# Optimization experiments

Hardware: AMD Instinct MI355X
Metric: run time of the kernel (lower is better)

The kernel has to match this reference:

```python
import jax, jax.numpy as jnp
import numpy as np

B, S, E = 2, 2048, 2048
H, KV, HD = 16, 4, 128  # num_heads, num_kv_heads, head_dim
G = H // KV             # query heads per kv head
ROPE_BASE = 10000.0


def rope_tables(dim, maxlen):
    freqs = 1.0 / ROPE_BASE ** (jnp.arange(0, dim, 2, dtype=jnp.float32) / dim)
    t = jnp.arange(maxlen, dtype=jnp.float32)
    f = jnp.outer(t, freqs)  # (maxlen, dim//2)
    return jnp.cos(f), jnp.sin(f)


def apply_rope(x, cos, sin):
    # x: (..., seq, heads, head_dim); interleaved-pair rotation
    s_len = x.shape[-3]
    c = cos[:s_len][:, None, :]
    s = sin[:s_len][:, None, :]
    x1 = x[..., ::2]
    x2 = x[..., 1::2]
    return jnp.stack([x1 * c - x2 * s, x1 * s + x2 * c], axis=-1).reshape(x.shape)


def setup_inputs() -> dict:
    key = jax.random.key(0)
    kx, kq, kk, kv, ko = jax.random.split(key, 5)
    x = jax.random.normal(kx, (B, S, E), dtype=jnp.float32)
    Wq = jax.random.normal(kq, (E, H * HD), dtype=jnp.float32) * 0.02
    Wk = jax.random.normal(kk, (E, KV * HD), dtype=jnp.float32) * 0.02
    Wv = jax.random.normal(kv, (E, KV * HD), dtype=jnp.float32) * 0.02
    Wo = jax.random.normal(ko, (H * HD, E), dtype=jnp.float32) * 0.02
    mask = jnp.tril(jnp.ones((S, S), dtype=bool))[None, None]  # causal (1,1,S,S)
    return {"x": x, "Wq": Wq, "Wk": Wk, "Wv": Wv, "Wo": Wo, "mask": mask}


def reference(x, Wq, Wk, Wv, Wo, mask):
    b, s, _ = x.shape
    cos, sin = rope_tables(HD, s)
    q = (x @ Wq).reshape(b, s, H, HD)
    k = (x @ Wk).reshape(b, s, KV, HD)
    v = (x @ Wv).reshape(b, s, KV, HD)
    q = apply_rope(q, cos, sin)
    k = apply_rope(k, cos, sin)
    if G > 1:
        k = jnp.repeat(k, G, axis=2)  # (b, s, H, HD)
        v = jnp.repeat(v, G, axis=2)
    q = jnp.transpose(q, (0, 2, 1, 3))  # (b, H, s, HD)
    k = jnp.transpose(k, (0, 2, 1, 3))
    v = jnp.transpose(v, (0, 2, 1, 3))
    scale = jnp.sqrt(jnp.float32(HD)).astype(q.dtype)
    scores = jnp.einsum("bhqd,bhkd->bhqk", q, k) / scale
    scores = jnp.where(mask, scores, jnp.finfo(scores.dtype).min)
    attn = jax.nn.softmax(scores, axis=-1)
    out = jnp.einsum("bhqk,bhkd->bhqd", attn, v)
    out = jnp.transpose(out, (0, 2, 1, 3)).reshape(b, s, H * HD)
    return out @ Wo
```

## Files before the change

### kernel.cpp

```cpp
#include <hip/hip_runtime.h>
#include <hip/hip_bf16.h>
#include <cstdint>

#define B_ 2
#define S_ 2048
#define E_ 2048
#define H_ 16
#define KV_ 4
#define HD_ 128
#define BS_ (B_*S_)
#define QKV_LD 3072
#define SM_SCALE 0.08838834764831845f
#define SC_LOG2E 0.1275424488538497f

typedef __attribute__((ext_vector_type(8))) __bf16 bf16x8;
typedef __attribute__((ext_vector_type(4))) float  floatx4;

__device__ __forceinline__ unsigned short f2bf(float f) {
  union { float f; unsigned u; } v; v.f = f;
  unsigned r = v.u + 0x7fffu + ((v.u >> 16) & 1u);
  return (unsigned short)(r >> 16);
}
__device__ __forceinline__ float bf2f(unsigned short u) {
  union { unsigned u; float f; } v; v.u = ((unsigned)u) << 16; return v.f;
}
__device__ __forceinline__ unsigned pack_bf16x2(float a, float b) {
  union { __hip_bfloat162 h; unsigned u; } v;
  v.h = __float22bfloat162_rn(make_float2(a, b));
  return v.u;
}

__device__ __forceinline__ void async_cp16(const void* g, void* l) {
  __builtin_amdgcn_global_load_lds(
      (const __attribute__((address_space(1))) void*)g,
      (__attribute__((address_space(3))) void*)l, 16, 0, 0);
}

__global__ __launch_bounds__(256)
void cvt_bf16(const float* __restrict__ src, unsigned short* __restrict__ dst,
              int n4) {
  int idx = blockIdx.x * 256 + threadIdx.x;
  if (idx >= n4) return;
  float4 v = *(const float4*)(src + (size_t)idx * 4);
  ushort4 o;
  o.x = f2bf(v.x); o.y = f2bf(v.y); o.z = f2bf(v.z); o.w = f2bf(v.w);
  *(ushort4*)(dst + (size_t)idx * 4) = o;
}

__global__ __launch_bounds__(256)
void cvt_bf16_t(const float* __restrict__ src, unsigned short* __restrict__ dst,
                int N, int dld, int noff) {
  __shared__ float tile[64 * 65];
  const int t = threadIdx.x;
  const int bk = blockIdx.y * 64, bn = blockIdx.x * 64;
  const int r = t >> 2, cg = t & 3;
#pragma unroll
  for (int i = 0; i < 4; ++i) {
    int c = cg * 16 + i * 4;
    float4 v = *(const float4*)(src + (size_t)(bk + r) * N + bn + c);
    tile[r * 65 + c] = v.x; tile[r * 65 + c + 1] = v.y;
    tile[r * 65 + c + 2] = v.z; tile[r * 65 + c + 3] = v.w;
  }
  __syncthreads();
  const int nl = t >> 2, kg = t & 3;
  union { unsigned short u[16]; uint4 q[2]; } o;
#pragma unroll
  for (int j = 0; j < 16; ++j)
    o.u[j] = f2bf(tile[(kg * 16 + j) * 65 + nl]);
  unsigned short* dp = dst + (size_t)(noff + bn + nl) * dld + bk + kg * 16;
  *(uint4*)(dp) = o.q[0];
  *(uint4*)(dp + 8) = o.q[1];
}

__global__ __launch_bounds__(256)
void rope_kernel(unsigned short* __restrict__ qkv) {
  const int PPR = 1280;
  int idx = blockIdx.x * 256 + threadIdx.x;
  if (idx >= BS_ * PPR) return;
  int row = idx / PPR, p = idx - row * PPR;
  int col = (p < 1024) ? (2 * p) : (2048 + 2 * (p - 1024));
  int d = p & 63;
  int s = row & (S_ - 1);
  float freq = expf(-(float)d * 0.14391156831212787f);
  float ang = (float)s * freq;
  float c = cosf(ang), sn = sinf(ang);
  unsigned short* ptr = qkv + (size_t)row * QKV_LD + col;
  float x1 = bf2f(ptr[0]), x2 = bf2f(ptr[1]);
  ptr[0] = f2bf(x1 * c - x2 * sn);
  ptr[1] = f2bf(x1 * sn + x2 * c);
}

__global__ __launch_bounds__(256)
void vtrans_kernel(const unsigned short* __restrict__ qkv,
                   unsigned short* __restrict__ vt) {
  __shared__ unsigned short tile[64 * 72];
  const int tid = threadIdx.x;
  const int s0 = blockIdx.x * 64;
  const int g = blockIdx.y >> 1;
  const int hh = (blockIdx.y & 1) * 64;
  const int b = g >> 2, kvh = g & 3;
#pragma unroll
  for (int i = 0; i < 2; ++i) {
    int chunk = tid + i * 256;
    int r = chunk >> 3, c = (chunk & 7) * 8;
    uint4 v = *(const uint4*)(qkv + (size_t)(b * S_ + s0 + r) * QKV_LD + 2560 + kvh * HD_ + hh + c);
    *(uint4*)(tile + r * 72 + c) = v;
  }
  __syncthreads();
#pragma unroll
  for (int i = 0; i < 2; ++i) {
    int chunk = tid + i * 256;
    int hdr = chunk >> 3, sc = (chunk & 7) * 8;
    union { unsigned short u[8]; uint4 v; } t;
#pragma unroll
    for (int j = 0; j < 8; ++j) t.u[j] = tile[(sc + j) * 72 + hdr];
    *(uint4*)(vt + (size_t)(g * HD_ + hh + hdr) * S_ + s0 + sc) = t.v;
  }
}

template<bool OUT_BF16>
__global__ __launch_bounds__(256, 2)
void gemm_tn(const unsigned short* __restrict__ A,
             const unsigned short* __restrict__ BT,
             void* __restrict__ C, int M, int N, int K) {
  __shared__ unsigned short Ash[128 * 32];
  __shared__ unsigned short Bsh[128 * 32];
  const int tid = threadIdx.x;
  const int l = tid & 63;
  const int l16 = l & 15, l4 = l >> 4;
  const int wave = tid >> 6;
  const int wm = (wave >> 1) * 64, wn = (wave & 1) * 64;
  const int bm = blockIdx.y * 128, bn = blockIdx.x * 128;

  const int srow = l >> 2;
  const int sg = (((l & 3) - (l >> 4)) & 3) * 8;

  floatx4 acc[4][4] = {};

  for (int kb = 0; kb < K; kb += 32) {
    __syncthreads();
#pragma unroll
    for (int i = 0; i < 2; ++i) {
      int cc = wave + i * 4;
      async_cp16(A + (size_t)(bm + 16 * cc + srow) * K + kb + sg, &Ash[cc * 512]);
      async_cp16(BT + (size_t)(bn + 16 * cc + srow) * K + kb + sg, &Bsh[cc * 512]);
    }
    __syncthreads();
    bf16x8 af[4], bf[4];
#pragma unroll
    for (int t = 0; t < 4; ++t) {
      int row = wm + t * 16 + l16;
      int s = (l4 + (l16 >> 2)) & 3;
      af[t] = *(const bf16x8*)(Ash + row * 32 + s * 8);
    }
#pragma unroll
    for (int t = 0; t < 4; ++t) {
      int row = wn + t * 16 + l16;
      int s = (l4 + (l16 >> 2)) & 3;
      bf[t] = *(const bf16x8*)(Bsh + row * 32 + s * 8);
    }
#pragma unroll
    for (int tm = 0; tm < 4; ++tm)
#pragma unroll
      for (int tn = 0; tn < 4; ++tn)
        acc[tm][tn] = __builtin_amdgcn_mfma_f32_16x16x32_bf16(af[tm], bf[tn], acc[tm][tn], 0, 0, 0);
  }
#pragma unroll
  for (int tm = 0; tm < 4; ++tm)
#pragma unroll
    for (int tn = 0; tn < 4; ++tn)
#pragma unroll
      for (int r = 0; r < 4; ++r) {
        int row = bm + wm + tm * 16 + l4 * 4 + r;
        int col = bn + wn + tn * 16 + l16;
        float v = acc[tm][tn][r];
        if (OUT_BF16) ((unsigned short*)C)[(size_t)row * N + col] = f2bf(v);
        else          ((float*)C)[(size_t)row * N + col] = v;
      }
}

__global__ __launch_bounds__(256, 2)
void gqa_attention(const unsigned short* __restrict__ qkv,
                   const unsigned short* __restrict__ vt,
                   unsigned short* __restrict__ out) {
  __shared__ unsigned short Ksh[2][32 * 128];
  __shared__ unsigned short Vsh[2][128 * 32];

  const int tid = threadIdx.x, l = tid & 63, wave = tid >> 6;
  const int l16 = l & 15, l4 = l >> 4;
  const int g = blockIdx.x, b = g >> 2, kvh = g & 3;
  const int h = kvh * 4 + wave;

  const int k_subrow = l >> 4;
  const int v_subrow = l >> 2;
  const int gv = (((l & 3) - (l >> 4)) & 3) * 8;

  const int t = 63 - (int)blockIdx.y;
  const int qt = t * 32;
  const int nch = t + 1;

  bf16x8 qfA[4], qfB[4];
  {
    const unsigned short* qpA = qkv + (size_t)(b * S_ + qt + l16) * QKV_LD + h * HD_;
    const unsigned short* qpB = qpA + (size_t)16 * QKV_LD;
#pragma unroll
    for (int c = 0; c < 4; ++c) {
      qfA[c] = *(const bf16x8*)(qpA + c * 32 + l4 * 8);
      qfB[c] = *(const bf16x8*)(qpB + c * 32 + l4 * 8);
    }
  }
  asm volatile("s_waitcnt vmcnt(0)" ::: "memory");

  const unsigned short* kp[2];
  const unsigned short* vp[2];
#pragma unroll
  for (int i = 0; i < 2; ++i) {
    int cc = wave + i * 4;
    int krow = 4 * cc + k_subrow;
    int gk = (((l & 15) - krow) & 15) * 8;
    kp[i] = qkv + (size_t)(b * S_ + krow) * QKV_LD + 2048 + kvh * HD_ + gk;
    vp[i] = vt + (size_t)(g * HD_ + 16 * cc + v_subrow) * S_ + gv;
  }

#pragma unroll
  for (int i = 0; i < 2; ++i) {
    int cc = wave + i * 4;
    async_cp16(kp[i], &Ksh[0][cc * 512]);
    async_cp16(vp[i], &Vsh[0][cc * 512]);
  }

  float lsumA = 0.f, lsumB = 0.f;
  floatx4 accA[8] = {}, accB[8] = {};

  for (int it = 0; it < nch; ++it) {
    const int cur = it & 1;
    asm volatile("s_barrier" ::: "memory");
    {
      const int kb2 = (it + 1 < nch) ? (it + 1) * 32 : 0;
      const int ko = kb2 * QKV_LD;
#pragma unroll
      for (int i = 0; i < 2; ++i) {
        int cc = wave + i * 4;
        async_cp16(kp[i] + ko, &Ksh[cur ^ 1][cc * 512]);
        async_cp16(vp[i] + kb2, &Vsh[cur ^ 1][cc * 512]);
      }
    }
    asm volatile("s_waitcnt vmcnt(4)\n\ts_barrier" ::: "memory");

    floatx4 saccA[2] = {}, saccB[2] = {};
    __builtin_amdgcn_s_setprio(1);
#pragma unroll
    for (int half = 0; half < 2; ++half) {
      int krow = half * 16 + l16;
#pragma unroll
      for (int c = 0; c < 4; ++c) {
        int s = (c * 4 + l4 + l16) & 15;
        bf16x8 kf = *(const bf16x8*)(&Ksh[cur][krow * 128 + s * 8]);
        saccA[half] = __builtin_amdgcn_mfma_f32_16x16x32_bf16(kf, qfA[c], saccA[half], 0, 0, 0);
        saccB[half] = __builtin_amdgcn_mfma_f32_16x16x32_bf16(kf, qfB[c], saccB[half], 0, 0, 0);
      }
    }
    __builtin_amdgcn_s_setprio(0);

    float pA[8], pB[8];
    if (it == nch - 1) {
#pragma unroll
      for (int half = 0; half < 2; ++half)
#pragma unroll
        for (int r = 0; r < 4; ++r) {
          int kk = half * 16 + l4 * 4 + r;
          float vA = fminf(saccA[half][r] * SC_LOG2E, 80.f);
          if (kk > l16) vA = -3e38f;
          float eA = exp2f(vA);
          pA[half * 4 + r] = eA; lsumA += eA;
          float vB = fminf(saccB[half][r] * SC_LOG2E, 80.f);
          if (half == 1 && (l4 * 4 + r) > l16) vB = -3e38f;
          float eB = exp2f(vB);
          pB[half * 4 + r] = eB; lsumB += eB;
        }
    } else {
#pragma unroll
      for (int half = 0; half < 2; ++half)
#pragma unroll
        for (int r = 0; r < 4; ++r) {
          float eA = exp2f(fminf(saccA[half][r] * SC_LOG2E, 80.f));
          pA[half * 4 + r] = eA; lsumA += eA;
          float eB = exp2f(fminf(saccB[half][r] * SC_LOG2E, 80.f));
          pB[half * 4 + r] = eB; lsumB += eB;
        }
    }

    unsigned a0 = pack_bf16x2(pA[0], pA[1]);
    unsigned a1 = pack_bf16x2(pA[2], pA[3]);
    unsigned a2 = pack_bf16x2(pA[4], pA[5]);
    unsigned a3 = pack_bf16x2(pA[6], pA[7]);
    asm("v_permlane32_swap_b32 %0, %1" : "+v"(a0), "+v"(a2));
    asm("v_permlane16_swap_b32 %0, %1" : "+v"(a0), "+v"(a2));
    asm("v_permlane32_swap_b32 %0, %1" : "+v"(a1), "+v"(a3));
    asm("v_permlane16_swap_b32 %0, %1" : "+v"(a1), "+v"(a3));
    unsigned b0 = pack_bf16x2(pB[0], pB[1]);
    unsigned b1 = pack_bf16x2(pB[2], pB[3]);
    unsigned b2 = pack_bf16x2(pB[4], pB[5]);
    unsigned b3 = pack_bf16x2(pB[6], pB[7]);
    asm("v_permlane32_swap_b32 %0, %1" : "+v"(b0), "+v"(b2));
    asm("v_permlane16_swap_b32 %0, %1" : "+v"(b0), "+v"(b2));
    asm("v_permlane32_swap_b32 %0, %1" : "+v"(b1), "+v"(b3));
    asm("v_permlane16_swap_b32 %0, %1" : "+v"(b1), "+v"(b3));
    union { unsigned w[4]; bf16x8 v8; } punA, punB;
    punA.w[0] = a0; punA.w[1] = a1; punA.w[2] = a2; punA.w[3] = a3;
    punB.w[0] = b0; punB.w[1] = b1; punB.w[2] = b2; punB.w[3] = b3;
    const bf16x8 pfA = punA.v8;
    const bf16x8 pfB = punB.v8;

    __builtin_amdgcn_s_setprio(1);
#pragma unroll
    for (int u = 0; u < 8; ++u) {
      int row = u * 16 + l16;
      int s = (l4 + (l16 >> 2)) & 3;
      bf16x8 vf = *(const bf16x8*)(&Vsh[cur][row * 32 + s * 8]);
      accA[u] = __builtin_amdgcn_mfma_f32_16x16x32_bf16(vf, pfA, accA[u], 0, 0, 0);
      accB[u] = __builtin_amdgcn_mfma_f32_16x16x32_bf16(vf, pfB, accB[u], 0, 0, 0);
    }
    __builtin_amdgcn_s_setprio(0);
  }

  lsumA += __shfl_xor(lsumA, 16, 64);
  lsumA += __shfl_xor(lsumA, 32, 64);
  lsumB += __shfl_xor(lsumB, 16, 64);
  lsumB += __shfl_xor(lsumB, 32, 64);
  float invA = 1.0f / lsumA;
  float invB = 1.0f / lsumB;
  unsigned short* opA = out + (size_t)(b * S_ + qt + l16) * 2048 + h * HD_;
  unsigned short* opB = opA + (size_t)16 * 2048;
#pragma unroll
  for (int u = 0; u < 8; ++u) {
    uint2 oA, oB;
    oA.x = pack_bf16x2(accA[u][0] * invA, accA[u][1] * invA);
    oA.y = pack_bf16x2(accA[u][2] * invA, accA[u][3] * invA);
    *(uint2*)(opA + u * 16 + l4 * 4) = oA;
    oB.x = pack_bf16x2(accB[u][0] * invB, accB[u][1] * invB);
    oB.y = pack_bf16x2(accB[u][2] * invB, accB[u][3] * invB);
    *(uint2*)(opB + u * 16 + l4 * 4) = oB;
  }
}

extern "C" void kernel_launch(void* const* d_in, const int* in_sizes, int n_in,
                              void* d_out, int out_size, void* d_ws, size_t ws_size,
                              hipStream_t stream) {
  const float* x  = (const float*)d_in[0];
  const float* Wq = (const float*)d_in[1];
  const float* Wk = (const float*)d_in[2];
  const float* Wv = (const float*)d_in[3];
  const float* Wo = (const float*)d_in[4];
  float* out = (float*)d_out;

  char* ws = (char*)d_ws;
  unsigned short* xb    = (unsigned short*)(ws);
  unsigned short* wqkvT = (unsigned short*)(ws + 16777216);
  unsigned short* woT   = (unsigned short*)(ws + 29360128);
  unsigned short* qkv   = (unsigned short*)(ws + 37748736);
  unsigned short* attn  = (unsigned short*)(ws + 62914560);
  unsigned short* vt    = (unsigned short*)(ws);

  cvt_bf16<<<(4096 * 2048 / 4 + 255) / 256, 256, 0, stream>>>(x, xb, 4096 * 2048 / 4);
  cvt_bf16_t<<<dim3(32, 32), 256, 0, stream>>>(Wq, wqkvT, 2048, 2048, 0);
  cvt_bf16_t<<<dim3(8, 32),  256, 0, stream>>>(Wk, wqkvT, 512,  2048, 2048);
  cvt_bf16_t<<<dim3(8, 32),  256, 0, stream>>>(Wv, wqkvT, 512,  2048, 2560);
  cvt_bf16_t<<<dim3(32, 32), 256, 0, stream>>>(Wo, woT,  2048, 2048, 0);

  gemm_tn<true><<<dim3(24, 32), 256, 0, stream>>>(xb, wqkvT, qkv, 4096, 3072, 2048);
  rope_kernel<<<(4096 * 1280 + 255) / 256, 256, 0, stream>>>(qkv);
  vtrans_kernel<<<dim3(32, 16), 256, 0, stream>>>(qkv, vt);
  gqa_attention<<<dim3(8, 64), 256, 0, stream>>>(qkv, vt, attn);
  gemm_tn<false><<<dim3(16, 32), 256, 0, stream>>>(attn, woT, out, 4096, 2048, 2048);
}
```

Before: 349.1 us.

## Pair causal query tiles per block and process 64-key chunks

Each attention block now handles two query tiles (y and 63-y) in sequence so causal work per block is balanced, and the grid shrinks to 256 blocks. The key loop advances in 64-key superchunks with doubled LDS buffers, which halves the barriers per key and issues more loads per stage. Launch bounds drop to one block per SM, and the s_setprio hints are removed. In exchange, fewer resident waves are available to hide latency, and 256 blocks may underfill the GPU.

```diff
diff --git a/kernel.cpp b/kernel.cpp
--- a/kernel.cpp
+++ b/kernel.cpp
@@ -179,37 +179,22 @@
       }
 }
 
-__global__ __launch_bounds__(256, 2)
+__global__ __launch_bounds__(256, 1)
 void gqa_attention(const unsigned short* __restrict__ qkv,
                    const unsigned short* __restrict__ vt,
                    unsigned short* __restrict__ out) {
-  __shared__ unsigned short Ksh[2][32 * 128];
-  __shared__ unsigned short Vsh[2][128 * 32];
+  __shared__ unsigned short Ksh[2][2 * 32 * 128];
+  __shared__ unsigned short Vsh[2][2 * 128 * 32];
 
   const int tid = threadIdx.x, l = tid & 63, wave = tid >> 6;
   const int l16 = l & 15, l4 = l >> 4;
   const int g = blockIdx.x, b = g >> 2, kvh = g & 3;
   const int h = kvh * 4 + wave;
+  const int y = blockIdx.y;
 
   const int k_subrow = l >> 4;
   const int v_subrow = l >> 2;
   const int gv = (((l & 3) - (l >> 4)) & 3) * 8;
-
-  const int t = 63 - (int)blockIdx.y;
-  const int qt = t * 32;
-  const int nch = t + 1;
-
-  bf16x8 qfA[4], qfB[4];
-  {
-    const unsigned short* qpA = qkv + (size_t)(b * S_ + qt + l16) * QKV_LD + h * HD_;
-    const unsigned short* qpB = qpA + (size_t)16 * QKV_LD;
-#pragma unroll
-    for (int c = 0; c < 4; ++c) {
-      qfA[c] = *(const bf16x8*)(qpA + c * 32 + l4 * 8);
-      qfB[c] = *(const bf16x8*)(qpB + c * 32 + l4 * 8);
-    }
-  }
-  asm volatile("s_waitcnt vmcnt(0)" ::: "memory");
 
   const unsigned short* kp[2];
   const unsigned short* vp[2];
@@ -222,125 +207,199 @@
     vp[i] = vt + (size_t)(g * HD_ + 16 * cc + v_subrow) * S_ + gv;
   }
 
-#pragma unroll
-  for (int i = 0; i < 2; ++i) {
-    int cc = wave + i * 4;
-    async_cp16(kp[i], &Ksh[0][cc * 512]);
-    async_cp16(vp[i], &Vsh[0][cc * 512]);
-  }
-
-  float lsumA = 0.f, lsumB = 0.f;
-  floatx4 accA[8] = {}, accB[8] = {};
-
-  for (int it = 0; it < nch; ++it) {
-    const int cur = it & 1;
+  for (int phase = 0; phase < 2; ++phase) {
+    const int t = phase ? (63 - y) : y;
+    const int qt = t * 32;
+    const int nsc = (t >> 1) + 1;
+    const bool todd = (t & 1) != 0;
+
+    bf16x8 qfA[4], qfB[4];
+    {
+      const unsigned short* qpA = qkv + (size_t)(b * S_ + qt + l16) * QKV_LD + h * HD_;
+      const unsigned short* qpB = qpA + (size_t)16 * QKV_LD;
+#pragma unroll
+      for (int c = 0; c < 4; ++c) {
+        qfA[c] = *(const bf16x8*)(qpA + c * 32 + l4 * 8);
+        qfB[c] = *(const bf16x8*)(qpB + c * 32 + l4 * 8);
+      }
+    }
+    asm volatile("s_waitcnt vmcnt(0)" ::: "memory");
     asm volatile("s_barrier" ::: "memory");
-    {
-      const int kb2 = (it + 1 < nch) ? (it + 1) * 32 : 0;
-      const int ko = kb2 * QKV_LD;
-#pragma unroll
-      for (int i = 0; i < 2; ++i) {
-        int cc = wave + i * 4;
-        async_cp16(kp[i] + ko, &Ksh[cur ^ 1][cc * 512]);
-        async_cp16(vp[i] + kb2, &Vsh[cur ^ 1][cc * 512]);
-      }
-    }
-    asm volatile("s_waitcnt vmcnt(4)\n\ts_barrier" ::: "memory");
-
-    floatx4 saccA[2] = {}, saccB[2] = {};
-    __builtin_amdgcn_s_setprio(1);
-#pragma unroll
-    for (int half = 0; half < 2; ++half) {
-      int krow = half * 16 + l16;
-#pragma unroll
-      for (int c = 0; c < 4; ++c) {
-        int s = (c * 4 + l4 + l16) & 15;
-        bf16x8 kf = *(const bf16x8*)(&Ksh[cur][krow * 128 + s * 8]);
-        saccA[half] = __builtin_amdgcn_mfma_f32_16x16x32_bf16(kf, qfA[c], saccA[half], 0, 0, 0);
-        saccB[half] = __builtin_amdgcn_mfma_f32_16x16x32_bf16(kf, qfB[c], saccB[half], 0, 0, 0);
-      }
-    }
-    __builtin_amdgcn_s_setprio(0);
-
-    float pA[8], pB[8];
-    if (it == nch - 1) {
-#pragma unroll
-      for (int half = 0; half < 2; ++half)
-#pragma unroll
-        for (int r = 0; r < 4; ++r) {
-          int kk = half * 16 + l4 * 4 + r;
-          float vA = fminf(saccA[half][r] * SC_LOG2E, 80.f);
-          if (kk > l16) vA = -3e38f;
-          float eA = exp2f(vA);
-          pA[half * 4 + r] = eA; lsumA += eA;
-          float vB = fminf(saccB[half][r] * SC_LOG2E, 80.f);
-          if (half == 1 && (l4 * 4 + r) > l16) vB = -3e38f;
-          float eB = exp2f(vB);
-          pB[half * 4 + r] = eB; lsumB += eB;
+
+#pragma unroll
+    for (int i = 0; i < 4; ++i) {
+      const int jj = i >> 1, ii = i & 1;
+      const int cc8 = wave + 4 * ii;
+      async_cp16(kp[ii] + jj * 32 * QKV_LD, &Ksh[0][jj * 4096 + cc8 * 512]);
+      async_cp16(vp[ii] + jj * 32,          &Vsh[0][jj * 4096 + cc8 * 512]);
+    }
+
+    float lsumA = 0.f, lsumB = 0.f;
+    floatx4 accA[8] = {}, accB[8] = {};
+
+    for (int it = 0; it < nsc; ++it) {
+      const int cur = it & 1;
+      asm volatile("s_barrier" ::: "memory");
+      {
+        const int kb2 = (it + 1 < nsc) ? (it + 1) * 64 : 0;
+        const int ko = kb2 * QKV_LD;
+#pragma unroll
+        for (int i = 0; i < 4; ++i) {
+          const int jj = i >> 1, ii = i & 1;
+          const int cc8 = wave + 4 * ii;
+          async_cp16(kp[ii] + ko + jj * 32 * QKV_LD, &Ksh[cur ^ 1][jj * 4096 + cc8 * 512]);
+          async_cp16(vp[ii] + kb2 + jj * 32,         &Vsh[cur ^ 1][jj * 4096 + cc8 * 512]);
         }
-    } else {
-#pragma unroll
-      for (int half = 0; half < 2; ++half)
-#pragma unroll
-        for (int r = 0; r < 4; ++r) {
-          float eA = exp2f(fminf(saccA[half][r] * SC_LOG2E, 80.f));
-          pA[half * 4 + r] = eA; lsumA += eA;
-          float eB = exp2f(fminf(saccB[half][r] * SC_LOG2E, 80.f));
-          pB[half * 4 + r] = eB; lsumB += eB;
+      }
+      asm volatile("s_waitcnt vmcnt(8)\n\ts_barrier" ::: "memory");
+
+      const bool last = (it == nsc - 1);
+      const bool skip1 = last && !todd;
+      const bool tri0 = last && !todd;
+      const bool tri1 = last && todd;
+
+      floatx4 sA[2][2] = {}, sB[2][2] = {};
+#pragma unroll
+      for (int half = 0; half < 2; ++half) {
+        const int krow = half * 16 + l16;
+#pragma unroll
+        for (int c = 0; c < 4; ++c) {
+          const int s = (c * 4 + l4 + l16) & 15;
+          bf16x8 kf = *(const bf16x8*)(&Ksh[cur][krow * 128 + s * 8]);
+          sA[0][half] = __builtin_amdgcn_mfma_f32_16x16x32_bf16(kf, qfA[c], sA[0][half], 0, 0, 0);
+          sB[0][half] = __builtin_amdgcn_mfma_f32_16x16x32_bf16(kf, qfB[c], sB[0][half], 0, 0, 0);
         }
-    }
-
-    unsigned a0 = pack_bf16x2(pA[0], pA[1]);
-    unsigned a1 = pack_bf16x2(pA[2], pA[3]);
-    unsigned a2 = pack_bf16x2(pA[4], pA[5]);
-    unsigned a3 = pack_bf16x2(pA[6], pA[7]);
-    asm("v_permlane32_swap_b32 %0, %1" : "+v"(a0), "+v"(a2));
-    asm("v_permlane16_swap_b32 %0, %1" : "+v"(a0), "+v"(a2));
-    asm("v_permlane32_swap_b32 %0, %1" : "+v"(a1), "+v"(a3));
-    asm("v_permlane16_swap_b32 %0, %1" : "+v"(a1), "+v"(a3));
-    unsigned b0 = pack_bf16x2(pB[0], pB[1]);
-    unsigned b1 = pack_bf16x2(pB[2], pB[3]);
-    unsigned b2 = pack_bf16x2(pB[4], pB[5]);
-    unsigned b3 = pack_bf16x2(pB[6], pB[7]);
-    asm("v_permlane32_swap_b32 %0, %1" : "+v"(b0), "+v"(b2));
-    asm("v_permlane16_swap_b32 %0, %1" : "+v"(b0), "+v"(b2));
-    asm("v_permlane32_swap_b32 %0, %1" : "+v"(b1), "+v"(b3));
-    asm("v_permlane16_swap_b32 %0, %1" : "+v"(b1), "+v"(b3));
-    union { unsigned w[4]; bf16x8 v8; } punA, punB;
-    punA.w[0] = a0; punA.w[1] = a1; punA.w[2] = a2; punA.w[3] = a3;
-    punB.w[0] = b0; punB.w[1] = b1; punB.w[2] = b2; punB.w[3] = b3;
-    const bf16x8 pfA = punA.v8;
-    const bf16x8 pfB = punB.v8;
-
-    __builtin_amdgcn_s_setprio(1);
+      }
+      if (!skip1) {
+#pragma unroll
+        for (int half = 0; half < 2; ++half) {
+          const int krow = half * 16 + l16;
+#pragma unroll
+          for (int c = 0; c < 4; ++c) {
+            const int s = (c * 4 + l4 + l16) & 15;
+            bf16x8 kf = *(const bf16x8*)(&Ksh[cur][4096 + krow * 128 + s * 8]);
+            sA[1][half] = __builtin_amdgcn_mfma_f32_16x16x32_bf16(kf, qfA[c], sA[1][half], 0, 0, 0);
+            sB[1][half] = __builtin_amdgcn_mfma_f32_16x16x32_bf16(kf, qfB[c], sB[1][half], 0, 0, 0);
+          }
+        }
+      }
+
+      bf16x8 pfA0, pfB0, pfA1, pfB1;
+      {
+        float pA[8], pB[8];
+#pragma unroll
+        for (int half = 0; half < 2; ++half)
+#pragma unroll
+          for (int r = 0; r < 4; ++r) {
+            float vA = fminf(sA[0][half][r] * SC_LOG2E, 80.f);
+            float vB = fminf(sB[0][half][r] * SC_LOG2E, 80.f);
+            if (tri0) {
+              int kk = half * 16 + l4 * 4 + r;
+              if (kk > l16) vA = -3e38f;
+              if (half == 1 && (l4 * 4 + r) > l16) vB = -3e38f;
+            }
+            float eA = exp2f(vA), eB = exp2f(vB);
+            pA[half * 4 + r] = eA; lsumA += eA;
+            pB[half * 4 + r] = eB; lsumB += eB;
+          }
+        unsigned a0 = pack_bf16x2(pA[0], pA[1]);
+        unsigned a1 = pack_bf16x2(pA[2], pA[3]);
+        unsigned a2 = pack_bf16x2(pA[4], pA[5]);
+        unsigned a3 = pack_bf16x2(pA[6], pA[7]);
+        asm("v_permlane32_swap_b32 %0, %1" : "+v"(a0), "+v"(a2));
+        asm("v_permlane16_swap_b32 %0, %1" : "+v"(a0), "+v"(a2));
+        asm("v_permlane32_swap_b32 %0, %1" : "+v"(a1), "+v"(a3));
+        asm("v_permlane16_swap_b32 %0, %1" : "+v"(a1), "+v"(a3));
+        unsigned b0 = pack_bf16x2(pB[0], pB[1]);
+        unsigned b1 = pack_bf16x2(pB[2], pB[3]);
+        unsigned b2 = pack_bf16x2(pB[4], pB[5]);
+        unsigned b3 = pack_bf16x2(pB[6], pB[7]);
+        asm("v_permlane32_swap_b32 %0, %1" : "+v"(b0), "+v"(b2));
+        asm("v_permlane16_swap_b32 %0, %1" : "+v"(b0), "+v"(b2));
+        asm("v_permlane32_swap_b32 %0, %1" : "+v"(b1), "+v"(b3));
+        asm("v_permlane16_swap_b32 %0, %1" : "+v"(b1), "+v"(b3));
+        union { unsigned w[4]; bf16x8 v8; } punA, punB;
+        punA.w[0] = a0; punA.w[1] = a1; punA.w[2] = a2; punA.w[3] = a3;
+        punB.w[0] = b0; punB.w[1] = b1; punB.w[2] = b2; punB.w[3] = b3;
+        pfA0 = punA.v8; pfB0 = punB.v8;
+      }
+      if (!skip1) {
+        float pA[8], pB[8];
+#pragma unroll
+        for (int half = 0; half < 2; ++half)
+#pragma unroll
+          for (int r = 0; r < 4; ++r) {
+            float vA = fminf(sA[1][half][r] * SC_LOG2E, 80.f);
+            float vB = fminf(sB[1][half][r] * SC_LOG2E, 80.f);
+            if (tri1) {
+              int kk = half * 16 + l4 * 4 + r;
+              if (kk > l16) vA = -3e38f;
+              if (half == 1 && (l4 * 4 + r) > l16) vB = -3e38f;
+            }
+            float eA = exp2f(vA), eB = exp2f(vB);
+            pA[half * 4 + r] = eA; lsumA += eA;
+            pB[half * 4 + r] = eB; lsumB += eB;
+          }
+        unsigned a0 = pack_bf16x2(pA[0], pA[1]);
+        unsigned a1 = pack_bf16x2(pA[2], pA[3]);
+        unsigned a2 = pack_bf16x2(pA[4], pA[5]);
+        unsigned a3 = pack_bf16x2(pA[6], pA[7]);
+        asm("v_permlane32_swap_b32 %0, %1" : "+v"(a0), "+v"(a2));
+        asm("v_permlane16_swap_b32 %0, %1" : "+v"(a0), "+v"(a2));
+        asm("v_permlane32_swap_b32 %0, %1" : "+v"(a1), "+v"(a3));
+        asm("v_permlane16_swap_b32 %0, %1" : "+v"(a1), "+v"(a3));
+        unsigned b0 = pack_bf16x2(pB[0], pB[1]);
+        unsigned b1 = pack_bf16x2(pB[2], pB[3]);
+        unsigned b2 = pack_bf16x2(pB[4], pB[5]);
+        unsigned b3 = pack_bf16x2(pB[6], pB[7]);
+        asm("v_permlane32_swap_b32 %0, %1" : "+v"(b0), "+v"(b2));
+        asm("v_permlane16_swap_b32 %0, %1" : "+v"(b0), "+v"(b2));
+        asm("v_permlane32_swap_b32 %0, %1" : "+v"(b1), "+v"(b3));
+        asm("v_permlane16_swap_b32 %0, %1" : "+v"(b1), "+v"(b3));
+        union { unsigned w[4]; bf16x8 v8; } punA, punB;
+        punA.w[0] = a0; punA.w[1] = a1; punA.w[2] = a2; punA.w[3] = a3;
+        punB.w[0] = b0; punB.w[1] = b1; punB.w[2] = b2; punB.w[3] = b3;
+        pfA1 = punA.v8; pfB1 = punB.v8;
+      }
+
+#pragma unroll
+      for (int u = 0; u < 8; ++u) {
+        const int row = u * 16 + l16;
+        const int s = (l4 + (l16 >> 2)) & 3;
+        bf16x8 vf = *(const bf16x8*)(&Vsh[cur][row * 32 + s * 8]);
+        accA[u] = __builtin_amdgcn_mfma_f32_16x16x32_bf16(vf, pfA0, accA[u], 0, 0, 0);
+        accB[u] = __builtin_amdgcn_mfma_f32_16x16x32_bf16(vf, pfB0, accB[u], 0, 0, 0);
+      }
+      if (!skip1) {
+#pragma unroll
+        for (int u = 0; u < 8; ++u) {
+          const int row = u * 16 + l16;
+          const int s = (l4 + (l16 >> 2)) & 3;
+          bf16x8 vf = *(const bf16x8*)(&Vsh[cur][4096 + row * 32 + s * 8]);
+          accA[u] = __builtin_amdgcn_mfma_f32_16x16x32_bf16(vf, pfA1, accA[u], 0, 0, 0);
+          accB[u] = __builtin_amdgcn_mfma_f32_16x16x32_bf16(vf, pfB1, accB[u], 0, 0, 0);
+        }
+      }
+    }
+
+    lsumA += __shfl_xor(lsumA, 16, 64);
+    lsumA += __shfl_xor(lsumA, 32, 64);
+    lsumB += __shfl_xor(lsumB, 16, 64);
+    lsumB += __shfl_xor(lsumB, 32, 64);
+    float invA = 1.0f / lsumA;
+    float invB = 1.0f / lsumB;
+    unsigned short* opA = out + (size_t)(b * S_ + qt + l16) * 2048 + h * HD_;
+    unsigned short* opB = opA + (size_t)16 * 2048;
 #pragma unroll
     for (int u = 0; u < 8; ++u) {
-      int row = u * 16 + l16;
-      int s = (l4 + (l16 >> 2)) & 3;
-      bf16x8 vf = *(const bf16x8*)(&Vsh[cur][row * 32 + s * 8]);
-      accA[u] = __builtin_amdgcn_mfma_f32_16x16x32_bf16(vf, pfA, accA[u], 0, 0, 0);
-      accB[u] = __builtin_amdgcn_mfma_f32_16x16x32_bf16(vf, pfB, accB[u], 0, 0, 0);
-    }
-    __builtin_amdgcn_s_setprio(0);
-  }
-
-  lsumA += __shfl_xor(lsumA, 16, 64);
-  lsumA += __shfl_xor(lsumA, 32, 64);
-  lsumB += __shfl_xor(lsumB, 16, 64);
-  lsumB += __shfl_xor(lsumB, 32, 64);
-  float invA = 1.0f / lsumA;
-  float invB = 1.0f / lsumB;
-  unsigned short* opA = out + (size_t)(b * S_ + qt + l16) * 2048 + h * HD_;
-  unsigned short* opB = opA + (size_t)16 * 2048;
-#pragma unroll
-  for (int u = 0; u < 8; ++u) {
-    uint2 oA, oB;
-    oA.x = pack_bf16x2(accA[u][0] * invA, accA[u][1] * invA);
-    oA.y = pack_bf16x2(accA[u][2] * invA, accA[u][3] * invA);
-    *(uint2*)(opA + u * 16 + l4 * 4) = oA;
-    oB.x = pack_bf16x2(accB[u][0] * invB, accB[u][1] * invB);
-    oB.y = pack_bf16x2(accB[u][2] * invB, accB[u][3] * invB);
-    *(uint2*)(opB + u * 16 + l4 * 4) = oB;
+      uint2 oA, oB;
+      oA.x = pack_bf16x2(accA[u][0] * invA, accA[u][1] * invA);
+      oA.y = pack_bf16x2(accA[u][2] * invA, accA[u][3] * invA);
+      *(uint2*)(opA + u * 16 + l4 * 4) = oA;
+      oB.x = pack_bf16x2(accB[u][0] * invB, accB[u][1] * invB);
+      oB.y = pack_bf16x2(accB[u][2] * invB, accB[u][3] * invB);
+      *(uint2*)(opB + u * 16 + l4 * 4) = oB;
+    }
   }
 }
 
@@ -371,6 +430,6 @@
   gemm_tn<true><<<dim3(24, 32), 256, 0, stream>>>(xb, wqkvT, qkv, 4096, 3072, 2048);
   rope_kernel<<<(4096 * 1280 + 255) / 256, 256, 0, stream>>>(qkv);
   vtrans_kernel<<<dim3(32, 16), 256, 0, stream>>>(qkv, vt);
-  gqa_attention<<<dim3(8, 64), 256, 0, stream>>>(qkv, vt, attn);
+  gqa_attention<<<dim3(8, 32), 256, 0, stream>>>(qkv, vt, attn);
   gemm_tn<false><<<dim3(16, 32), 256, 0, stream>>>(attn, woT, out, 4096, 2048, 2048);
 }
```

Result: no change. 347.3 us (-0.5%).

## Split KV range across two wave groups and pair causal query tiles per block

Applied to the files above, without the earlier changes.

Each attention block now runs 512 threads: two groups of four waves split the KV chunks of a query tile and merge partial accumulators and row sums through shared memory. Each block processes two query tiles (y and 63-y), which balances the causal workload across the grid, now halved to 8x32 blocks. The split is meant to raise parallelism inside each tile and cut per-block tail imbalance. In exchange it adds a shared-memory reduction with four extra barriers per tile, doubles the LDS buffers, and idles some seg-0 steps when the chunk count is odd.

```diff
diff --git a/kernel.cpp b/kernel.cpp
--- a/kernel.cpp
+++ b/kernel.cpp
@@ -179,168 +179,203 @@
       }
 }
 
-__global__ __launch_bounds__(256, 2)
+__global__ __launch_bounds__(512, 2)
 void gqa_attention(const unsigned short* __restrict__ qkv,
                    const unsigned short* __restrict__ vt,
                    unsigned short* __restrict__ out) {
-  __shared__ unsigned short Ksh[2][32 * 128];
-  __shared__ unsigned short Vsh[2][128 * 32];
+  __shared__ unsigned short Ksh[2][2][32 * 128];
+  __shared__ unsigned short Vsh[2][2][128 * 32];
 
   const int tid = threadIdx.x, l = tid & 63, wave = tid >> 6;
   const int l16 = l & 15, l4 = l >> 4;
+  const int hw = wave & 3, seg = wave >> 2;
   const int g = blockIdx.x, b = g >> 2, kvh = g & 3;
-  const int h = kvh * 4 + wave;
+  const int h = kvh * 4 + hw;
+  const int y = blockIdx.y;
 
   const int k_subrow = l >> 4;
   const int v_subrow = l >> 2;
   const int gv = (((l & 3) - (l >> 4)) & 3) * 8;
 
-  const int t = 63 - (int)blockIdx.y;
-  const int qt = t * 32;
-  const int nch = t + 1;
-
-  bf16x8 qfA[4], qfB[4];
-  {
-    const unsigned short* qpA = qkv + (size_t)(b * S_ + qt + l16) * QKV_LD + h * HD_;
-    const unsigned short* qpB = qpA + (size_t)16 * QKV_LD;
-#pragma unroll
-    for (int c = 0; c < 4; ++c) {
-      qfA[c] = *(const bf16x8*)(qpA + c * 32 + l4 * 8);
-      qfB[c] = *(const bf16x8*)(qpB + c * 32 + l4 * 8);
-    }
-  }
-  asm volatile("s_waitcnt vmcnt(0)" ::: "memory");
-
   const unsigned short* kp[2];
   const unsigned short* vp[2];
 #pragma unroll
   for (int i = 0; i < 2; ++i) {
-    int cc = wave + i * 4;
+    int cc = hw + i * 4;
     int krow = 4 * cc + k_subrow;
     int gk = (((l & 15) - krow) & 15) * 8;
     kp[i] = qkv + (size_t)(b * S_ + krow) * QKV_LD + 2048 + kvh * HD_ + gk;
     vp[i] = vt + (size_t)(g * HD_ + 16 * cc + v_subrow) * S_ + gv;
   }
 
-#pragma unroll
-  for (int i = 0; i < 2; ++i) {
-    int cc = wave + i * 4;
-    async_cp16(kp[i], &Ksh[0][cc * 512]);
-    async_cp16(vp[i], &Vsh[0][cc * 512]);
-  }
-
-  float lsumA = 0.f, lsumB = 0.f;
-  floatx4 accA[8] = {}, accB[8] = {};
-
-  for (int it = 0; it < nch; ++it) {
-    const int cur = it & 1;
+  for (int phase = 0; phase < 2; ++phase) {
+    const int t = phase ? (63 - y) : y;
+    const int qt = t * 32;
+    const int nch = t + 1;
+    const int c0 = nch >> 1;
+    const int st = nch - c0;
+
+    bf16x8 qfA[4], qfB[4];
+    {
+      const unsigned short* qpA = qkv + (size_t)(b * S_ + qt + l16) * QKV_LD + h * HD_;
+      const unsigned short* qpB = qpA + (size_t)16 * QKV_LD;
+#pragma unroll
+      for (int c = 0; c < 4; ++c) {
+        qfA[c] = *(const bf16x8*)(qpA + c * 32 + l4 * 8);
+        qfB[c] = *(const bf16x8*)(qpB + c * 32 + l4 * 8);
+      }
+    }
+    asm volatile("s_waitcnt vmcnt(0)" ::: "memory");
     asm volatile("s_barrier" ::: "memory");
+
     {
-      const int kb2 = (it + 1 < nch) ? (it + 1) * 32 : 0;
-      const int ko = kb2 * QKV_LD;
+      const int ci = (seg == 0) ? 0 : c0;
+      const int ko = ci * 32 * QKV_LD, vo = ci * 32;
 #pragma unroll
       for (int i = 0; i < 2; ++i) {
-        int cc = wave + i * 4;
-        async_cp16(kp[i] + ko, &Ksh[cur ^ 1][cc * 512]);
-        async_cp16(vp[i] + kb2, &Vsh[cur ^ 1][cc * 512]);
-      }
-    }
-    asm volatile("s_waitcnt vmcnt(4)\n\ts_barrier" ::: "memory");
-
-    floatx4 saccA[2] = {}, saccB[2] = {};
-    __builtin_amdgcn_s_setprio(1);
-#pragma unroll
-    for (int half = 0; half < 2; ++half) {
-      int krow = half * 16 + l16;
-#pragma unroll
-      for (int c = 0; c < 4; ++c) {
-        int s = (c * 4 + l4 + l16) & 15;
-        bf16x8 kf = *(const bf16x8*)(&Ksh[cur][krow * 128 + s * 8]);
-        saccA[half] = __builtin_amdgcn_mfma_f32_16x16x32_bf16(kf, qfA[c], saccA[half], 0, 0, 0);
-        saccB[half] = __builtin_amdgcn_mfma_f32_16x16x32_bf16(kf, qfB[c], saccB[half], 0, 0, 0);
-      }
-    }
-    __builtin_amdgcn_s_setprio(0);
-
-    float pA[8], pB[8];
-    if (it == nch - 1) {
-#pragma unroll
-      for (int half = 0; half < 2; ++half)
-#pragma unroll
-        for (int r = 0; r < 4; ++r) {
-          int kk = half * 16 + l4 * 4 + r;
-          float vA = fminf(saccA[half][r] * SC_LOG2E, 80.f);
-          if (kk > l16) vA = -3e38f;
-          float eA = exp2f(vA);
-          pA[half * 4 + r] = eA; lsumA += eA;
-          float vB = fminf(saccB[half][r] * SC_LOG2E, 80.f);
-          if (half == 1 && (l4 * 4 + r) > l16) vB = -3e38f;
-          float eB = exp2f(vB);
-          pB[half * 4 + r] = eB; lsumB += eB;
+        int cc = hw + i * 4;
+        async_cp16(kp[i] + ko, &Ksh[seg][0][cc * 512]);
+        async_cp16(vp[i] + vo, &Vsh[seg][0][cc * 512]);
+      }
+    }
+
+    float lsumA = 0.f, lsumB = 0.f;
+    floatx4 accA[8] = {}, accB[8] = {};
+
+    for (int step = 0; step < st; ++step) {
+      const int cur = step & 1;
+      asm volatile("s_barrier" ::: "memory");
+      {
+        const int cn = step + 1;
+        const int cnext = (seg == 0) ? ((cn < c0) ? cn : 0)
+                                     : ((cn < st) ? (c0 + cn) : 0);
+        const int ko = cnext * 32 * QKV_LD, vo = cnext * 32;
+#pragma unroll
+        for (int i = 0; i < 2; ++i) {
+          int cc = hw + i * 4;
+          async_cp16(kp[i] + ko, &Ksh[seg][cur ^ 1][cc * 512]);
+          async_cp16(vp[i] + vo, &Vsh[seg][cur ^ 1][cc * 512]);
         }
-    } else {
-#pragma unroll
-      for (int half = 0; half < 2; ++half)
-#pragma unroll
-        for (int r = 0; r < 4; ++r) {
-          float eA = exp2f(fminf(saccA[half][r] * SC_LOG2E, 80.f));
-          pA[half * 4 + r] = eA; lsumA += eA;
-          float eB = exp2f(fminf(saccB[half][r] * SC_LOG2E, 80.f));
-          pB[half * 4 + r] = eB; lsumB += eB;
+      }
+      asm volatile("s_waitcnt vmcnt(4)\n\ts_barrier" ::: "memory");
+
+      const bool active = (seg == 1) || (step < c0);
+      if (active) {
+        const bool tri = (seg == 1) && (step == st - 1);
+
+        floatx4 sA[2] = {}, sB[2] = {};
+#pragma unroll
+        for (int half = 0; half < 2; ++half) {
+          const int krow = half * 16 + l16;
+#pragma unroll
+          for (int c = 0; c < 4; ++c) {
+            const int s = (c * 4 + l4 + l16) & 15;
+            bf16x8 kf = *(const bf16x8*)(&Ksh[seg][cur][krow * 128 + s * 8]);
+            sA[half] = __builtin_amdgcn_mfma_f32_16x16x32_bf16(kf, qfA[c], sA[half], 0, 0, 0);
+            sB[half] = __builtin_amdgcn_mfma_f32_16x16x32_bf16(kf, qfB[c], sB[half], 0, 0, 0);
+          }
         }
-    }
-
-    unsigned a0 = pack_bf16x2(pA[0], pA[1]);
-    unsigned a1 = pack_bf16x2(pA[2], pA[3]);
-    unsigned a2 = pack_bf16x2(pA[4], pA[5]);
-    unsigned a3 = pack_bf16x2(pA[6], pA[7]);
-    asm("v_permlane32_swap_b32 %0, %1" : "+v"(a0), "+v"(a2));
-    asm("v_permlane16_swap_b32 %0, %1" : "+v"(a0), "+v"(a2));
-    asm("v_permlane32_swap_b32 %0, %1" : "+v"(a1), "+v"(a3));
-    asm("v_permlane16_swap_b32 %0, %1" : "+v"(a1), "+v"(a3));
-    unsigned b0 = pack_bf16x2(pB[0], pB[1]);
-    unsigned b1 = pack_bf16x2(pB[2], pB[3]);
-    unsigned b2 = pack_bf16x2(pB[4], pB[5]);
-    unsigned b3 = pack_bf16x2(pB[6], pB[7]);
-    asm("v_permlane32_swap_b32 %0, %1" : "+v"(b0), "+v"(b2));
-    asm("v_permlane16_swap_b32 %0, %1" : "+v"(b0), "+v"(b2));
-    asm("v_permlane32_swap_b32 %0, %1" : "+v"(b1), "+v"(b3));
-    asm("v_permlane16_swap_b32 %0, %1" : "+v"(b1), "+v"(b3));
-    union { unsigned w[4]; bf16x8 v8; } punA, punB;
-    punA.w[0] = a0; punA.w[1] = a1; punA.w[2] = a2; punA.w[3] = a3;
-    punB.w[0] = b0; punB.w[1] = b1; punB.w[2] = b2; punB.w[3] = b3;
-    const bf16x8 pfA = punA.v8;
-    const bf16x8 pfB = punB.v8;
-
-    __builtin_amdgcn_s_setprio(1);
-#pragma unroll
-    for (int u = 0; u < 8; ++u) {
-      int row = u * 16 + l16;
-      int s = (l4 + (l16 >> 2)) & 3;
-      bf16x8 vf = *(const bf16x8*)(&Vsh[cur][row * 32 + s * 8]);
-      accA[u] = __builtin_amdgcn_mfma_f32_16x16x32_bf16(vf, pfA, accA[u], 0, 0, 0);
-      accB[u] = __builtin_amdgcn_mfma_f32_16x16x32_bf16(vf, pfB, accB[u], 0, 0, 0);
-    }
-    __builtin_amdgcn_s_setprio(0);
-  }
-
-  lsumA += __shfl_xor(lsumA, 16, 64);
-  lsumA += __shfl_xor(lsumA, 32, 64);
-  lsumB += __shfl_xor(lsumB, 16, 64);
-  lsumB += __shfl_xor(lsumB, 32, 64);
-  float invA = 1.0f / lsumA;
-  float invB = 1.0f / lsumB;
-  unsigned short* opA = out + (size_t)(b * S_ + qt + l16) * 2048 + h * HD_;
-  unsigned short* opB = opA + (size_t)16 * 2048;
-#pragma unroll
-  for (int u = 0; u < 8; ++u) {
-    uint2 oA, oB;
-    oA.x = pack_bf16x2(accA[u][0] * invA, accA[u][1] * invA);
-    oA.y = pack_bf16x2(accA[u][2] * invA, accA[u][3] * invA);
-    *(uint2*)(opA + u * 16 + l4 * 4) = oA;
-    oB.x = pack_bf16x2(accB[u][0] * invB, accB[u][1] * invB);
-    oB.y = pack_bf16x2(accB[u][2] * invB, accB[u][3] * invB);
-    *(uint2*)(opB + u * 16 + l4 * 4) = oB;
+
+        float pA[8], pB[8];
+#pragma unroll
+        for (int half = 0; half < 2; ++half)
+#pragma unroll
+          for (int r = 0; r < 4; ++r) {
+            float vA = fminf(sA[half][r] * SC_LOG2E, 80.f);
+            float vB = fminf(sB[half][r] * SC_LOG2E, 80.f);
+            if (tri) {
+              int kk = half * 16 + l4 * 4 + r;
+              if (kk > l16) vA = -3e38f;
+              if (half == 1 && (l4 * 4 + r) > l16) vB = -3e38f;
+            }
+            float eA = exp2f(vA), eB = exp2f(vB);
+            pA[half * 4 + r] = eA; lsumA += eA;
+            pB[half * 4 + r] = eB; lsumB += eB;
+          }
+
+        unsigned a0 = pack_bf16x2(pA[0], pA[1]);
+        unsigned a1 = pack_bf16x2(pA[2], pA[3]);
+        unsigned a2 = pack_bf16x2(pA[4], pA[5]);
+        unsigned a3 = pack_bf16x2(pA[6], pA[7]);
+        asm("v_permlane32_swap_b32 %0, %1" : "+v"(a0), "+v"(a2));
+        asm("v_permlane16_swap_b32 %0, %1" : "+v"(a0), "+v"(a2));
+        asm("v_permlane32_swap_b32 %0, %1" : "+v"(a1), "+v"(a3));
+        asm("v_permlane16_swap_b32 %0, %1" : "+v"(a1), "+v"(a3));
+        unsigned b0 = pack_bf16x2(pB[0], pB[1]);
+        unsigned b1 = pack_bf16x2(pB[2], pB[3]);
+        unsigned b2 = pack_bf16x2(pB[4], pB[5]);
+        unsigned b3 = pack_bf16x2(pB[6], pB[7]);
+        asm("v_permlane32_swap_b32 %0, %1" : "+v"(b0), "+v"(b2));
+        asm("v_permlane16_swap_b32 %0, %1" : "+v"(b0), "+v"(b2));
+        asm("v_permlane32_swap_b32 %0, %1" : "+v"(b1), "+v"(b3));
+        asm("v_permlane16_swap_b32 %0, %1" : "+v"(b1), "+v"(b3));
+        union { unsigned w[4]; bf16x8 v8; } punA, punB;
+        punA.w[0] = a0; punA.w[1] = a1; punA.w[2] = a2; punA.w[3] = a3;
+        punB.w[0] = b0; punB.w[1] = b1; punB.w[2] = b2; punB.w[3] = b3;
+        const bf16x8 pfA = punA.v8;
+        const bf16x8 pfB = punB.v8;
+
+#pragma unroll
+        for (int u = 0; u < 8; ++u) {
+          const int row = u * 16 + l16;
+          const int s = (l4 + (l16 >> 2)) & 3;
+          bf16x8 vf = *(const bf16x8*)(&Vsh[seg][cur][row * 32 + s * 8]);
+          accA[u] = __builtin_amdgcn_mfma_f32_16x16x32_bf16(vf, pfA, accA[u], 0, 0, 0);
+          accB[u] = __builtin_amdgcn_mfma_f32_16x16x32_bf16(vf, pfB, accB[u], 0, 0, 0);
+        }
+      }
+    }
+
+    asm volatile("s_waitcnt vmcnt(0)" ::: "memory");
+    __syncthreads();
+    float* combA = (float*)(&Ksh[0][0][0]);
+    float* combL = (float*)(&Vsh[0][0][0]);
+    if (seg == 1) {
+#pragma unroll
+      for (int u = 0; u < 8; ++u)
+        *(floatx4*)(combA + ((hw * 8 + u) * 64 + l) * 4) = accA[u];
+      combL[(hw * 64 + l) * 2]     = lsumA;
+      combL[(hw * 64 + l) * 2 + 1] = lsumB;
+    }
+    __syncthreads();
+    if (seg == 0) {
+#pragma unroll
+      for (int u = 0; u < 8; ++u)
+        accA[u] += *(const floatx4*)(combA + ((hw * 8 + u) * 64 + l) * 4);
+      lsumA += combL[(hw * 64 + l) * 2];
+      lsumB += combL[(hw * 64 + l) * 2 + 1];
+    }
+    __syncthreads();
+    if (seg == 1) {
+#pragma unroll
+      for (int u = 0; u < 8; ++u)
+        *(floatx4*)(combA + ((hw * 8 + u) * 64 + l) * 4) = accB[u];
+    }
+    __syncthreads();
+    if (seg == 0) {
+#pragma unroll
+      for (int u = 0; u < 8; ++u)
+        accB[u] += *(const floatx4*)(combA + ((hw * 8 + u) * 64 + l) * 4);
+
+      lsumA += __shfl_xor(lsumA, 16, 64);
+      lsumA += __shfl_xor(lsumA, 32, 64);
+      lsumB += __shfl_xor(lsumB, 16, 64);
+      lsumB += __shfl_xor(lsumB, 32, 64);
+      float invA = 1.0f / lsumA;
+      float invB = 1.0f / lsumB;
+      unsigned short* opA = out + (size_t)(b * S_ + qt + l16) * 2048 + h * HD_;
+      unsigned short* opB = opA + (size_t)16 * 2048;
+#pragma unroll
+      for (int u = 0; u < 8; ++u) {
+        uint2 oA, oB;
+        oA.x = pack_bf16x2(accA[u][0] * invA, accA[u][1] * invA);
+        oA.y = pack_bf16x2(accA[u][2] * invA, accA[u][3] * invA);
+        *(uint2*)(opA + u * 16 + l4 * 4) = oA;
+        oB.x = pack_bf16x2(accB[u][0] * invB, accB[u][1] * invB);
+        oB.y = pack_bf16x2(accB[u][2] * invB, accB[u][3] * invB);
+        *(uint2*)(opB + u * 16 + l4 * 4) = oB;
+      }
+    }
   }
 }
 
@@ -371,6 +406,6 @@
   gemm_tn<true><<<dim3(24, 32), 256, 0, stream>>>(xb, wqkvT, qkv, 4096, 3072, 2048);
   rope_kernel<<<(4096 * 1280 + 255) / 256, 256, 0, stream>>>(qkv);
   vtrans_kernel<<<dim3(32, 16), 256, 0, stream>>>(qkv, vt);
-  gqa_attention<<<dim3(8, 64), 256, 0, stream>>>(qkv, vt, attn);
+  gqa_attention<<<dim3(8, 32), 512, 0, stream>>>(qkv, vt, attn);
   gemm_tn<false><<<dim3(16, 32), 256, 0, stream>>>(attn, woT, out, 4096, 2048, 2048);
 }
```

After: 338.0 us, median of 2. 3.2% less time.
